# Kernel optimization log

Hardware: AMD Instinct MI355X
Metric: run time of the kernel (lower is better)

The kernel has to match this reference:

```python
import jax, jax.numpy as jnp
import numpy as np

D_MODEL = 1024
N_HEADS = 16
D_K = D_MODEL // N_HEADS
THETA = 10000.0


def _rope(x, token_positions):
    # x: [b, h, s, d_k]; interleaved RoPE (pairs at even/odd positions)
    half = D_K // 2
    inv_freq = 1.0 / (THETA ** (2.0 * jnp.arange(half, dtype=jnp.float32) / D_K))  # [half]
    angles = token_positions.astype(jnp.float32)[:, None] * inv_freq[None, :]      # [s, half]
    sin, cos = jnp.sin(angles), jnp.cos(angles)
    x_even = x[..., 0::2]
    x_odd = x[..., 1::2]
    out_even = cos * x_even - sin * x_odd
    out_odd = sin * x_even + cos * x_odd
    # interleave back: [..., half, 2] -> [..., d_k]
    return jnp.stack((out_even, out_odd), axis=-1).reshape(x.shape)


def setup_inputs() -> dict:
    key = jax.random.key(0)
    kx, kq, kk, kv, ko = jax.random.split(key, 5)
    b, s = 4, 2048
    std = (2.0 / (D_MODEL + D_MODEL)) ** 0.5
    return {
        "x": jax.random.normal(kx, (b, s, D_MODEL), dtype=jnp.float32),
        "Wq": jax.random.normal(kq, (D_MODEL, D_MODEL), dtype=jnp.float32) * std,
        "Wk": jax.random.normal(kk, (D_MODEL, D_MODEL), dtype=jnp.float32) * std,
        "Wv": jax.random.normal(kv, (D_MODEL, D_MODEL), dtype=jnp.float32) * std,
        "Wo": jax.random.normal(ko, (D_MODEL, D_MODEL), dtype=jnp.float32) * std,
        "token_positions": jnp.arange(s, dtype=jnp.int32),
    }


def reference(x, Wq, Wk, Wv, Wo, token_positions):
    b, s, _ = x.shape
    split = lambda t: t.reshape(b, s, N_HEADS, D_K).transpose(0, 2, 1, 3)  # b h s d
    q = split(x @ Wq.T)
    k = split(x @ Wk.T)
    v = split(x @ Wv.T)
    q = _rope(q, token_positions)
    k = _rope(k, token_positions)
    scores = jnp.einsum("bhnd,bhmd->bhnm", q, k) / jnp.sqrt(jnp.float32(D_K))
    causal = jnp.tril(jnp.ones((s, s), dtype=bool))
    scores = jnp.where(causal, scores, -jnp.inf)
    attn = jax.nn.softmax(scores, axis=-1)
    out = jnp.einsum("bhnm,bhmd->bhnd", attn, v)
    out = out.transpose(0, 2, 1, 3).reshape(b, s, D_MODEL)
    return out @ Wo.T
```

## Files before the change

### kernel.cpp

```cpp
#include <hip/hip_runtime.h>
#include <stdint.h>

typedef __attribute__((ext_vector_type(8))) __bf16 bf16x8;
typedef __attribute__((ext_vector_type(4))) float f32x4;
typedef __attribute__((ext_vector_type(16))) float f32x16;
typedef __attribute__((ext_vector_type(8))) unsigned short ushort8;

__device__ __forceinline__ unsigned short f2bf(float f){
  union { float f; unsigned int i; } v; v.f = f;
  unsigned int r = v.i + 0x7fffu + ((v.i >> 16) & 1u);
  return (unsigned short)(r >> 16);
}
__device__ __forceinline__ void gload16(const void* g, void* l){
  __builtin_amdgcn_global_load_lds((__attribute__((address_space(1))) void*)(g),
                                   (__attribute__((address_space(3))) void*)(l),
                                   16, 0, 0);
}
__device__ __forceinline__ unsigned int cvtpk(float lo, float hi){
  unsigned int r;
  asm("v_cvt_pk_bf16_f32 %0, %1, %2" : "=v"(r) : "v"(lo), "v"(hi));
  return r;
}
__device__ __forceinline__ float fexp2(float x){
  float r; asm("v_exp_f32 %0, %1" : "=v"(r) : "v"(x)); return r;
}
__device__ __forceinline__ bf16x8 ldsw(const char* tile, int row, int colb){
  return *(const bf16x8*)(tile + row*128 + (colb ^ ((row & 7) << 4)));
}

#define SEQ   2048
#define DM    1024
#define NH    16
#define DK    64
#define BATCH 4
#define MTOT  (BATCH*SEQ)
#define NX    (MTOT*DM)
#define NW    (DM*DM)

#define QSCALE 0.18033688011112f

__global__ __launch_bounds__(256) void k_tables(const int* __restrict__ pos,
                                                float* __restrict__ tab)
{
  const int idx = blockIdx.x * 256 + threadIdx.x;
  const int s = idx >> 5, i = idx & 31;
  const float inv = __expf(-0.28782313662425575f * (float)i);
  const float a = (float)pos[s] * inv;
  tab[2*idx]   = cosf(a);
  tab[2*idx+1] = sinf(a);
}

__global__ __launch_bounds__(256) void k_convert(
    const float* __restrict__ x,  const float* __restrict__ wq,
    const float* __restrict__ wk, const float* __restrict__ wv,
    const float* __restrict__ wo,
    unsigned short* __restrict__ xb, unsigned short* __restrict__ wb)
{
  const int tid = blockIdx.x * 256 + threadIdx.x;
  const long long e = (long long)tid * 8;
  const float* src; unsigned short* dst;
  if (e < NX) { src = x + e; dst = xb + e; }
  else {
    long long j = e - NX;
    int seg = (int)(j >> 20);
    long long off = j & 1048575;
    src = (seg==0?wq:seg==1?wk:seg==2?wv:wo) + off;
    dst = wb + (size_t)seg*NW + off;
  }
  const float4 a = *(const float4*)src;
  const float4 b = *(const float4*)(src + 4);
  uint4 o;
  o.x = (unsigned int)f2bf(a.x) | ((unsigned int)f2bf(a.y) << 16);
  o.y = (unsigned int)f2bf(a.z) | ((unsigned int)f2bf(a.w) << 16);
  o.z = (unsigned int)f2bf(b.x) | ((unsigned int)f2bf(b.y) << 16);
  o.w = (unsigned int)f2bf(b.z) | ((unsigned int)f2bf(b.w) << 16);
  *(uint4*)dst = o;
}

#define BK64 64
#define NT   (DM/BK64)
#define ABUF 32768
#define BSTRIDE 49152

template<int MODE>
__global__ __launch_bounds__(512, 2) void k_gemm(
    const unsigned short* __restrict__ A,
    const unsigned short* __restrict__ Wb,
    unsigned short* __restrict__ D0,
    unsigned short* __restrict__ D1,
    unsigned short* __restrict__ D2,
    float* __restrict__ Dout,
    const float* __restrict__ tab)
{
  __shared__ __attribute__((aligned(16))) char lds_[3*BSTRIDE];
  const int tid  = threadIdx.x;
  const int lane = tid & 63;
  const int w    = tid >> 6;
  const int wm = w >> 1, wn = w & 1;

  const int bid = blockIdx.x;
  const int tq  = bid >> 3;
  const int m0  = ((bid & 7)*4 + (tq & 3)) * 256;
  const int r   = tq >> 2;
  const int n0  = (MODE == 0 ? (r & 7) : r) * 128;
  const int z   = (MODE == 0) ? (r >> 3) : 0;

  const unsigned short* W = Wb + (size_t)z * NW;
  unsigned short* Dh = (MODE == 0) ? ((z == 0) ? D0 : (z == 1) ? D1 : D2) : nullptr;
  const bool vtr = (MODE == 0) && (z == 2);

  f32x4 acc[4][4];
  #pragma unroll
  for (int i = 0; i < 4; ++i)
    #pragma unroll
    for (int j = 0; j < 4; ++j)
      acc[i][j] = (f32x4)0.0f;

  auto stA = [&](int buf, int t, int l){
    const int k0 = t * BK64;
    const int id = l*512 + tid;
    const int row = id >> 3, c = id & 7;
    gload16(A + (size_t)(m0 + row)*DM + k0 + ((c ^ (row & 7)) << 3),
            lds_ + buf*BSTRIDE + id*16);
  };
  auto stB = [&](int buf, int t, int l){
    const int k0 = t * BK64;
    const int id = l*512 + tid;
    const int row = id >> 3, c = id & 7;
    gload16(W + (size_t)(n0 + row)*DM + k0 + ((c ^ (row & 7)) << 3),
            lds_ + buf*BSTRIDE + ABUF + id*16);
  };
  auto ldA = [&](const char* Ab_, int i, int kk){
    const int row = wm*64 + i*16 + (lane & 15);
    const int c = (kk*4 + (lane >> 4)) ^ (row & 7);
    return *(const bf16x8*)(Ab_ + row*128 + (c << 4));
  };
  auto ldB = [&](const char* Bb_, int j, int kk){
    const int row = wn*64 + j*16 + (lane & 15);
    const int c = (kk*4 + (lane >> 4)) ^ (row & 7);
    return *(const bf16x8*)(Bb_ + row*128 + (c << 4));
  };

  #pragma unroll
  for (int l = 0; l < 4; ++l) stA(0, 0, l);
  stB(0, 0, 0); stB(0, 0, 1);
  #pragma unroll
  for (int l = 0; l < 4; ++l) stA(1, 1, l);
  stB(1, 1, 0); stB(1, 1, 1);
  asm volatile("s_waitcnt vmcnt(6)" ::: "memory");
  __builtin_amdgcn_s_barrier();

  int rb = 0, sb = 2;
  for (int t = 0; t < NT; ++t){
    const char* Ab_ = lds_ + rb*BSTRIDE;
    const char* Bb_ = Ab_ + ABUF;
    const bool st = (t + 2 < NT);
    bf16x8 aF0, aF1, bF[4];

    aF0 = ldA(Ab_, 0, 0); aF1 = ldA(Ab_, 1, 0);
    bF[0] = ldB(Bb_, 0, 0); bF[1] = ldB(Bb_, 1, 0);
    bF[2] = ldB(Bb_, 2, 0); bF[3] = ldB(Bb_, 3, 0);
    if (st){ stA(sb, t+2, 0); stA(sb, t+2, 1); }
    __builtin_amdgcn_s_barrier();
    asm volatile("s_waitcnt lgkmcnt(0)" ::: "memory");
    __builtin_amdgcn_s_setprio(1);
    #pragma unroll
    for (int j = 0; j < 4; ++j){
      acc[0][j] = __builtin_amdgcn_mfma_f32_16x16x32_bf16(aF0, bF[j], acc[0][j], 0, 0, 0);
      acc[1][j] = __builtin_amdgcn_mfma_f32_16x16x32_bf16(aF1, bF[j], acc[1][j], 0, 0, 0);
    }
    __builtin_amdgcn_s_setprio(0);
    __builtin_amdgcn_s_barrier();

    aF0 = ldA(Ab_, 2, 0); aF1 = ldA(Ab_, 3, 0);
    if (st){ stA(sb, t+2, 2); stA(sb, t+2, 3); }
    __builtin_amdgcn_s_barrier();
    asm volatile("s_waitcnt lgkmcnt(0)" ::: "memory");
    __builtin_amdgcn_s_setprio(1);
    #pragma unroll
    for (int j = 0; j < 4; ++j){
      acc[2][j] = __builtin_amdgcn_mfma_f32_16x16x32_bf16(aF0, bF[j], acc[2][j], 0, 0, 0);
      acc[3][j] = __builtin_amdgcn_mfma_f32_16x16x32_bf16(aF1, bF[j], acc[3][j], 0, 0, 0);
    }
    __builtin_amdgcn_s_setprio(0);
    __builtin_amdgcn_s_barrier();

    aF0 = ldA(Ab_, 0, 1); aF1 = ldA(Ab_, 1, 1);
    bF[0] = ldB(Bb_, 0, 1); bF[1] = ldB(Bb_, 1, 1);
    bF[2] = ldB(Bb_, 2, 1); bF[3] = ldB(Bb_, 3, 1);
    if (st){ stB(sb, t+2, 0); stB(sb, t+2, 1); }
    __builtin_amdgcn_s_barrier();
    asm volatile("s_waitcnt lgkmcnt(0)" ::: "memory");
    __builtin_amdgcn_s_setprio(1);
    #pragma unroll
    for (int j = 0; j < 4; ++j){
      acc[0][j] = __builtin_amdgcn_mfma_f32_16x16x32_bf16(aF0, bF[j], acc[0][j], 0, 0, 0);
      acc[1][j] = __builtin_amdgcn_mfma_f32_16x16x32_bf16(aF1, bF[j], acc[1][j], 0, 0, 0);
    }
    __builtin_amdgcn_s_setprio(0);
    __builtin_amdgcn_s_barrier();

    aF0 = ldA(Ab_, 2, 1); aF1 = ldA(Ab_, 3, 1);
    __builtin_amdgcn_s_barrier();
    asm volatile("s_waitcnt lgkmcnt(0)" ::: "memory");
    __builtin_amdgcn_s_setprio(1);
    #pragma unroll
    for (int j = 0; j < 4; ++j){
      acc[2][j] = __builtin_amdgcn_mfma_f32_16x16x32_bf16(aF0, bF[j], acc[2][j], 0, 0, 0);
      acc[3][j] = __builtin_amdgcn_mfma_f32_16x16x32_bf16(aF1, bF[j], acc[3][j], 0, 0, 0);
    }
    __builtin_amdgcn_s_setprio(0);
    if (t < NT-2)       asm volatile("s_waitcnt vmcnt(6)" ::: "memory");
    else if (t == NT-2) asm volatile("s_waitcnt vmcnt(0)" ::: "memory");
    if (t < NT-1) __builtin_amdgcn_s_barrier();

    rb = (rb == 2) ? 0 : rb + 1;
    sb = (sb == 2) ? 0 : sb + 1;
  }

  __syncthreads();

  {
    float* T = (float*)lds_;
    #pragma unroll
    for (int i = 0; i < 4; ++i)
      #pragma unroll
      for (int j = 0; j < 4; ++j){
        const int n = wn*64 + j*16 + (lane & 15);
        #pragma unroll
        for (int rr = 0; rr < 4; ++rr){
          const int m = wm*64 + i*16 + ((lane >> 4) << 2) + rr;
          T[m*128 + (n ^ ((m & 7) << 2))] = acc[i][j][rr];
        }
      }
  }
  __syncthreads();
  const float* T = (const float*)lds_;

  if (MODE == 0 && vtr){
    const int nl = tid >> 2;
    const int sblk = tid & 3;
    const int d = nl & 63, hh = (n0 >> 6) + (nl >> 6);
    const int bidx = m0 >> 11;
    unsigned short* vrow = Dh + (((size_t)(bidx*NH + hh))*DK + d)*SEQ + (m0 & 2047);
    #pragma unroll
    for (int c = 0; c < 8; ++c){
      const int s0 = sblk*8 + c*32;
      float v[8];
      #pragma unroll
      for (int j2 = 0; j2 < 8; ++j2)
        v[j2] = T[(s0 + j2)*128 + (nl ^ (((s0 + j2) & 7) << 2))];
      uint4 ov;
      ov.x = cvtpk(v[0], v[1]); ov.y = cvtpk(v[2], v[3]);
      ov.z = cvtpk(v[4], v[5]); ov.w = cvtpk(v[6], v[7]);
      *(uint4*)(vrow + s0) = ov;
    }
  } else {
    const float scale = (MODE == 0 && z == 0) ? QSCALE : 1.0f;
    #pragma unroll
    for (int k = 0; k < 8; ++k){
      const int cid = k*512 + tid;
      const int d8   = cid & 7;
      const int sp_l = (cid >> 3) & 255;
      const int h    = cid >> 11;
      const int nb   = h*64 + d8*8;
      const int sw   = (sp_l & 7) << 2;
      const f32x4 c0 = *(const f32x4*)&T[sp_l*128 + (nb ^ sw)];
      const f32x4 c1 = *(const f32x4*)&T[sp_l*128 + ((nb + 4) ^ sw)];
      if (MODE == 1){
        float* dst = Dout + (size_t)(m0 + sp_l)*DM + n0 + nb;
        *(f32x4*)dst = c0;
        *(f32x4*)(dst + 4) = c1;
      } else {
        const int mg = m0 + sp_l;
        const int bidx = mg >> 11, sp = mg & 2047;
        const float4 t01 = *(const float4*)&tab[(size_t)sp*64 + d8*8];
        const float4 t23 = *(const float4*)&tab[(size_t)sp*64 + d8*8 + 4];
        const unsigned int u0 = cvtpk((t01.x*c0[0] - t01.y*c0[1])*scale,
                                      (t01.y*c0[0] + t01.x*c0[1])*scale);
        const unsigned int u1 = cvtpk((t01.z*c0[2] - t01.w*c0[3])*scale,
                                      (t01.w*c0[2] + t01.z*c0[3])*scale);
        const unsigned int u2 = cvtpk((t23.x*c1[0] - t23.y*c1[1])*scale,
                                      (t23.y*c1[0] + t23.x*c1[1])*scale);
        const unsigned int u3 = cvtpk((t23.z*c1[2] - t23.w*c1[3])*scale,
                                      (t23.w*c1[2] + t23.z*c1[3])*scale);
        const int hh = (n0 >> 6) + h;
        uint4 ov; ov.x = u0; ov.y = u1; ov.z = u2; ov.w = u3;
        *(uint4*)(Dh + ((size_t)((bidx*NH + hh)*SEQ + sp))*DK + d8*8) = ov;
      }
    }
  }
}

__global__ __launch_bounds__(512, 4) void k_attn(const unsigned short* __restrict__ Qh,
                                                 const unsigned short* __restrict__ Kh,
                                                 const unsigned short* __restrict__ Vt,
                                                 unsigned short* __restrict__ Ab)
{
  __shared__ uint4 ldsu[4096];
  char* base = (char*)ldsu;
  const int tid  = threadIdx.x;
  const int lane = tid & 63;
  const int w    = tid >> 6;
  const int ww   = w & 3;
  const int g    = w >> 2;
  const int tl   = tid & 255;
  const int l31  = lane & 31;
  const int hl   = lane >> 5;
  char* gb = base + g*32768;

  const int jj = blockIdx.x, bh = blockIdx.y;
  const unsigned short* Qb = Qh + (size_t)bh*(SEQ*DK);
  const unsigned short* Kb = Kh + (size_t)bh*(SEQ*DK);
  const unsigned short* Vb = Vt + (size_t)bh*(SEQ*DK);
  const int b = bh >> 4, hd = bh & 15;

  for (int pass = 0; pass < 2; ++pass){
    const int qt = pass ? jj : 15 - jj;
    const int q0 = qt * 128;
    const int qbase = q0 + ww*32;

    bf16x8 qf[4];
    #pragma unroll
    for (int t = 0; t < 4; ++t)
      qf[t] = *(const bf16x8*)(Qb + (size_t)(qbase + l31)*DK + t*16 + hl*8);

    f32x16 acc0 = (f32x16)0.0f, acc1 = (f32x16)0.0f;
    float lsum = 0.0f;

    const int nk = qt + 1;
    const int tbase = g * nk;
    const int wqmax = qbase + 31;

    auto stage = [&](int buf, int ktile){
      const int k0s = ktile * 64;
      char* Kd = gb + buf*16384;
      char* Vd = Kd + 8192;
      #pragma unroll
      for (int cc = 0; cc < 2; ++cc){
        const int f = cc*256 + tl;
        const int r = f >> 3, slot = f & 7;
        const int sw = ((slot ^ (r & 7)) << 3);
        gload16(Kb + (size_t)(k0s + r)*DK + sw, Kd + (cc*256 + ww*64)*16);
        gload16(Vb + (size_t)r*SEQ + k0s + sw, Vd + (cc*256 + ww*64)*16);
      }
    };

    if (pass) __syncthreads();
    stage(0, tbase);
    __syncthreads();
    int cur = 0;

    for (int kt = 0; kt < nk; ++kt){
      const int k0 = (tbase + kt) * 64;
      if (kt + 1 < nk) stage(cur ^ 1, tbase + kt + 1);
      if (k0 <= wqmax){
        const char* Ks = gb + cur*16384;
        const char* Vs = Ks + 8192;

        f32x16 sv0 = (f32x16)0.0f, sv1 = (f32x16)0.0f;
        __builtin_amdgcn_s_setprio(1);
        #pragma unroll
        for (int t = 0; t < 4; ++t){
          const int colb = t*32 + hl*16;
          const bf16x8 a0 = ldsw(Ks, l31, colb);
          const bf16x8 a1 = ldsw(Ks, 32 + l31, colb);
          sv0 = __builtin_amdgcn_mfma_f32_32x32x16_bf16(a0, qf[t], sv0, 0, 0, 0);
          sv1 = __builtin_amdgcn_mfma_f32_32x32x16_bf16(a1, qf[t], sv1, 0, 0, 0);
        }
        __builtin_amdgcn_s_setprio(0);

        if (k0 + 63 > qbase){
          const int q = qbase + l31;
          #pragma unroll
          for (int j = 0; j < 16; ++j){
            const int kv = k0 + (j&3) + 8*(j>>2) + 4*hl;
            if (kv > q)      sv0[j] = -1e30f;
            if (kv + 32 > q) sv1[j] = -1e30f;
          }
        }

        #pragma unroll
        for (int j = 0; j < 16; ++j){
          sv0[j] = fexp2(sv0[j]);
          sv1[j] = fexp2(sv1[j]);
        }
        float ts[8];
        #pragma unroll
        for (int j = 0; j < 8; ++j)
          ts[j] = (sv0[j] + sv0[j+8]) + (sv1[j] + sv1[j+8]);
        #pragma unroll
        for (int off = 4; off; off >>= 1)
          #pragma unroll
          for (int j = 0; j < off; ++j)
            ts[j] += ts[j+off];
        lsum += ts[0] + __shfl_xor(ts[0], 32, 64);

        __builtin_amdgcn_s_setprio(1);
        #pragma unroll
        for (int t = 0; t < 4; ++t){
          f32x16& s = (t < 2) ? sv0 : sv1;
          const int b0v = (t & 1) * 8;
          const unsigned int A0 = cvtpk(s[b0v+0], s[b0v+1]);
          const unsigned int A1 = cvtpk(s[b0v+2], s[b0v+3]);
          const unsigned int B0 = cvtpk(s[b0v+4], s[b0v+5]);
          const unsigned int B1 = cvtpk(s[b0v+6], s[b0v+7]);
          const unsigned int s0 = hl ? A0 : B0;
          const unsigned int s1 = hl ? A1 : B1;
          const unsigned int r0 = (unsigned int)__shfl_xor((int)s0, 32, 64);
          const unsigned int r1 = (unsigned int)__shfl_xor((int)s1, 32, 64);
          union { unsigned int u[4]; bf16x8 v; } f;
          f.u[0] = hl ? r0 : A0; f.u[1] = hl ? r1 : A1;
          f.u[2] = hl ? B0 : r0; f.u[3] = hl ? B1 : r1;
          const int colb = t*32 + hl*16;
          const bf16x8 v0 = ldsw(Vs, l31, colb);
          const bf16x8 v1 = ldsw(Vs, 32 + l31, colb);
          acc0 = __builtin_amdgcn_mfma_f32_32x32x16_bf16(v0, f.v, acc0, 0, 0, 0);
          acc1 = __builtin_amdgcn_mfma_f32_32x32x16_bf16(v1, f.v, acc1, 0, 0, 0);
        }
        __builtin_amdgcn_s_setprio(0);
      }
      __syncthreads();
      cur ^= 1;
    }

    if (g == 1){
      char* cw = base + ww*9216 + lane*144;
      #pragma unroll
      for (int q4 = 0; q4 < 4; ++q4){
        *(f32x4*)(cw + q4*16)      = (f32x4){acc0[4*q4], acc0[4*q4+1], acc0[4*q4+2], acc0[4*q4+3]};
        *(f32x4*)(cw + 64 + q4*16) = (f32x4){acc1[4*q4], acc1[4*q4+1], acc1[4*q4+2], acc1[4*q4+3]};
      }
      *(float*)(cw + 128) = lsum;
    }
    __syncthreads();
    if (g == 0){
      const char* cr = base + ww*9216 + lane*144;
      const float l1 = *(const float*)(cr + 128);
      const float linv = 1.0f / (lsum + l1);
      unsigned short* orow = Ab + ((size_t)(b*SEQ + qbase + l31))*DM + hd*DK;
      #pragma unroll
      for (int mt = 0; mt < 2; ++mt){
        #pragma unroll
        for (int g4 = 0; g4 < 4; ++g4){
          const f32x16& a = mt ? acc1 : acc0;
          const f32x4 o = *(const f32x4*)(cr + mt*64 + g4*16);
          const unsigned int u0 = cvtpk((a[4*g4+0] + o[0])*linv, (a[4*g4+1] + o[1])*linv);
          const unsigned int u1 = cvtpk((a[4*g4+2] + o[2])*linv, (a[4*g4+3] + o[3])*linv);
          *(unsigned long long*)(orow + mt*32 + g4*8 + hl*4) =
              (unsigned long long)u0 | ((unsigned long long)u1 << 32);
        }
      }
    }
  }
}

extern "C" void kernel_launch(void* const* d_in, const int* in_sizes, int n_in,
                              void* d_out, int out_size, void* d_ws, size_t ws_size,
                              hipStream_t stream)
{
  (void)in_sizes; (void)n_in; (void)out_size;
  const float* x  = (const float*)d_in[0];
  const float* wq = (const float*)d_in[1];
  const float* wk = (const float*)d_in[2];
  const float* wv = (const float*)d_in[3];
  const float* wo = (const float*)d_in[4];
  const int* pos  = (const int*)d_in[5];
  float* out = (float*)d_out;

  if (ws_size < 92800000u) return;
  char* ws = (char*)d_ws;
  unsigned short* xb = (unsigned short*)(ws);
  unsigned short* wb = (unsigned short*)(ws + 16777216);
  unsigned short* Qh = (unsigned short*)(ws + 25165824);
  unsigned short* Kh = (unsigned short*)(ws + 41943040);
  unsigned short* Vt = (unsigned short*)(ws + 75497472);
  float* tab         = (float*)(ws + 92274688);

  k_tables  <<<256, 256, 0, stream>>>(pos, tab);
  k_convert <<<6144, 256, 0, stream>>>(x, wq, wk, wv, wo, xb, wb);
  k_gemm<0> <<<768, 512, 0, stream>>>(xb, wb, Qh, Kh, Vt, nullptr, tab);
  k_attn    <<<dim3(8, 64), 512, 0, stream>>>(Qh, Kh, Vt, xb);
  k_gemm<1> <<<256, 512, 0, stream>>>(xb, wb + 3*NW, nullptr, nullptr,
                                      nullptr, out, nullptr);
}
```

Measured before the change: 164.6 us.

## Use larger 256x256 tiles with double buffering for fused QKV projection GEMM

Splits the QKV projection into a dedicated kernel that computes 256x256 output tiles per block with 8 waves in a 2x4 layout. Each wave now holds 8x4 accumulators and the K loop is double-buffered over 128 KB of LDS instead of triple-buffered, which halves the block count to 384 and raises arithmetic intensity per global load. The epilogue is done in two halves to fit the transposed tile in LDS. The costs are one block per CU, higher register pressure and fewer blocks than the 256-CU machine can fill evenly, with a full vmcnt(0) wait each iteration.

```diff
diff --git a/kernel.cpp b/kernel.cpp
--- a/kernel.cpp
+++ b/kernel.cpp
@@ -77,61 +77,55 @@
   *(uint4*)dst = o;
 }
 
-#define BK64 64
-#define NT   (DM/BK64)
-#define ABUF 32768
-#define BSTRIDE 49152
-
-template<int MODE>
-__global__ __launch_bounds__(512, 2) void k_gemm(
+#define G0_NT 16
+#define G0_BSTR 65536
+
+__global__ __launch_bounds__(512) void k_g0(
     const unsigned short* __restrict__ A,
     const unsigned short* __restrict__ Wb,
     unsigned short* __restrict__ D0,
     unsigned short* __restrict__ D1,
     unsigned short* __restrict__ D2,
-    float* __restrict__ Dout,
     const float* __restrict__ tab)
 {
-  __shared__ __attribute__((aligned(16))) char lds_[3*BSTRIDE];
+  __shared__ __attribute__((aligned(16))) char lds_[131072];
   const int tid  = threadIdx.x;
   const int lane = tid & 63;
   const int w    = tid >> 6;
-  const int wm = w >> 1, wn = w & 1;
+  const int wm = w >> 2, wn = w & 3;
 
   const int bid = blockIdx.x;
   const int tq  = bid >> 3;
   const int m0  = ((bid & 7)*4 + (tq & 3)) * 256;
   const int r   = tq >> 2;
-  const int n0  = (MODE == 0 ? (r & 7) : r) * 128;
-  const int z   = (MODE == 0) ? (r >> 3) : 0;
+  const int n0  = (r & 3) * 256;
+  const int z   = r >> 2;
 
   const unsigned short* W = Wb + (size_t)z * NW;
-  unsigned short* Dh = (MODE == 0) ? ((z == 0) ? D0 : (z == 1) ? D1 : D2) : nullptr;
-  const bool vtr = (MODE == 0) && (z == 2);
-
-  f32x4 acc[4][4];
-  #pragma unroll
-  for (int i = 0; i < 4; ++i)
+  unsigned short* Dh = (z == 0) ? D0 : (z == 1) ? D1 : D2;
+  const bool vtr = (z == 2);
+
+  f32x4 acc[8][4];
+  #pragma unroll
+  for (int i = 0; i < 8; ++i)
     #pragma unroll
     for (int j = 0; j < 4; ++j)
       acc[i][j] = (f32x4)0.0f;
 
   auto stA = [&](int buf, int t, int l){
-    const int k0 = t * BK64;
     const int id = l*512 + tid;
     const int row = id >> 3, c = id & 7;
-    gload16(A + (size_t)(m0 + row)*DM + k0 + ((c ^ (row & 7)) << 3),
-            lds_ + buf*BSTRIDE + id*16);
+    gload16(A + (size_t)(m0 + row)*DM + t*64 + ((c ^ (row & 7)) << 3),
+            lds_ + buf*G0_BSTR + id*16);
   };
   auto stB = [&](int buf, int t, int l){
-    const int k0 = t * BK64;
     const int id = l*512 + tid;
     const int row = id >> 3, c = id & 7;
-    gload16(W + (size_t)(n0 + row)*DM + k0 + ((c ^ (row & 7)) << 3),
-            lds_ + buf*BSTRIDE + ABUF + id*16);
+    gload16(W + (size_t)(n0 + row)*DM + t*64 + ((c ^ (row & 7)) << 3),
+            lds_ + buf*G0_BSTR + 32768 + id*16);
   };
   auto ldA = [&](const char* Ab_, int i, int kk){
-    const int row = wm*64 + i*16 + (lane & 15);
+    const int row = wm*128 + i*16 + (lane & 15);
     const int c = (kk*4 + (lane >> 4)) ^ (row & 7);
     return *(const bf16x8*)(Ab_ + row*128 + (c << 4));
   };
@@ -141,141 +135,126 @@
     return *(const bf16x8*)(Bb_ + row*128 + (c << 4));
   };
 
+#define G0_MFMA16(IA, IB)                                                               \
+  _Pragma("unroll")                                                                     \
+  for (int j = 0; j < 4; ++j){                                                          \
+    acc[IA][j] = __builtin_amdgcn_mfma_f32_16x16x32_bf16(aF[0][0], bF[j][0], acc[IA][j], 0, 0, 0); \
+    acc[IA][j] = __builtin_amdgcn_mfma_f32_16x16x32_bf16(aF[0][1], bF[j][1], acc[IA][j], 0, 0, 0); \
+    acc[IB][j] = __builtin_amdgcn_mfma_f32_16x16x32_bf16(aF[1][0], bF[j][0], acc[IB][j], 0, 0, 0); \
+    acc[IB][j] = __builtin_amdgcn_mfma_f32_16x16x32_bf16(aF[1][1], bF[j][1], acc[IB][j], 0, 0, 0); \
+  }
+
   #pragma unroll
   for (int l = 0; l < 4; ++l) stA(0, 0, l);
-  stB(0, 0, 0); stB(0, 0, 1);
-  #pragma unroll
-  for (int l = 0; l < 4; ++l) stA(1, 1, l);
-  stB(1, 1, 0); stB(1, 1, 1);
-  asm volatile("s_waitcnt vmcnt(6)" ::: "memory");
+  #pragma unroll
+  for (int l = 0; l < 4; ++l) stB(0, 0, l);
+  asm volatile("s_waitcnt vmcnt(0)" ::: "memory");
   __builtin_amdgcn_s_barrier();
 
-  int rb = 0, sb = 2;
-  for (int t = 0; t < NT; ++t){
-    const char* Ab_ = lds_ + rb*BSTRIDE;
-    const char* Bb_ = Ab_ + ABUF;
-    const bool st = (t + 2 < NT);
-    bf16x8 aF0, aF1, bF[4];
-
-    aF0 = ldA(Ab_, 0, 0); aF1 = ldA(Ab_, 1, 0);
-    bF[0] = ldB(Bb_, 0, 0); bF[1] = ldB(Bb_, 1, 0);
-    bF[2] = ldB(Bb_, 2, 0); bF[3] = ldB(Bb_, 3, 0);
-    if (st){ stA(sb, t+2, 0); stA(sb, t+2, 1); }
-    __builtin_amdgcn_s_barrier();
-    asm volatile("s_waitcnt lgkmcnt(0)" ::: "memory");
-    __builtin_amdgcn_s_setprio(1);
-    #pragma unroll
-    for (int j = 0; j < 4; ++j){
-      acc[0][j] = __builtin_amdgcn_mfma_f32_16x16x32_bf16(aF0, bF[j], acc[0][j], 0, 0, 0);
-      acc[1][j] = __builtin_amdgcn_mfma_f32_16x16x32_bf16(aF1, bF[j], acc[1][j], 0, 0, 0);
-    }
-    __builtin_amdgcn_s_setprio(0);
-    __builtin_amdgcn_s_barrier();
-
-    aF0 = ldA(Ab_, 2, 0); aF1 = ldA(Ab_, 3, 0);
-    if (st){ stA(sb, t+2, 2); stA(sb, t+2, 3); }
-    __builtin_amdgcn_s_barrier();
-    asm volatile("s_waitcnt lgkmcnt(0)" ::: "memory");
-    __builtin_amdgcn_s_setprio(1);
-    #pragma unroll
-    for (int j = 0; j < 4; ++j){
-      acc[2][j] = __builtin_amdgcn_mfma_f32_16x16x32_bf16(aF0, bF[j], acc[2][j], 0, 0, 0);
-      acc[3][j] = __builtin_amdgcn_mfma_f32_16x16x32_bf16(aF1, bF[j], acc[3][j], 0, 0, 0);
-    }
-    __builtin_amdgcn_s_setprio(0);
-    __builtin_amdgcn_s_barrier();
-
-    aF0 = ldA(Ab_, 0, 1); aF1 = ldA(Ab_, 1, 1);
-    bF[0] = ldB(Bb_, 0, 1); bF[1] = ldB(Bb_, 1, 1);
-    bF[2] = ldB(Bb_, 2, 1); bF[3] = ldB(Bb_, 3, 1);
-    if (st){ stB(sb, t+2, 0); stB(sb, t+2, 1); }
-    __builtin_amdgcn_s_barrier();
-    asm volatile("s_waitcnt lgkmcnt(0)" ::: "memory");
-    __builtin_amdgcn_s_setprio(1);
-    #pragma unroll
-    for (int j = 0; j < 4; ++j){
-      acc[0][j] = __builtin_amdgcn_mfma_f32_16x16x32_bf16(aF0, bF[j], acc[0][j], 0, 0, 0);
-      acc[1][j] = __builtin_amdgcn_mfma_f32_16x16x32_bf16(aF1, bF[j], acc[1][j], 0, 0, 0);
-    }
-    __builtin_amdgcn_s_setprio(0);
-    __builtin_amdgcn_s_barrier();
-
-    aF0 = ldA(Ab_, 2, 1); aF1 = ldA(Ab_, 3, 1);
-    __builtin_amdgcn_s_barrier();
-    asm volatile("s_waitcnt lgkmcnt(0)" ::: "memory");
-    __builtin_amdgcn_s_setprio(1);
-    #pragma unroll
-    for (int j = 0; j < 4; ++j){
-      acc[2][j] = __builtin_amdgcn_mfma_f32_16x16x32_bf16(aF0, bF[j], acc[2][j], 0, 0, 0);
-      acc[3][j] = __builtin_amdgcn_mfma_f32_16x16x32_bf16(aF1, bF[j], acc[3][j], 0, 0, 0);
-    }
-    __builtin_amdgcn_s_setprio(0);
-    if (t < NT-2)       asm volatile("s_waitcnt vmcnt(6)" ::: "memory");
-    else if (t == NT-2) asm volatile("s_waitcnt vmcnt(0)" ::: "memory");
-    if (t < NT-1) __builtin_amdgcn_s_barrier();
-
-    rb = (rb == 2) ? 0 : rb + 1;
-    sb = (sb == 2) ? 0 : sb + 1;
-  }
+  for (int t = 0; t < G0_NT; ++t){
+    const char* Ab_ = lds_ + (t & 1)*G0_BSTR;
+    const char* Bb_ = Ab_ + 32768;
+    const int nb = (t + 1) & 1;
+    const bool st = (t + 1 < G0_NT);
+    bf16x8 aF[2][2], bF[4][2];
+
+    aF[0][0] = ldA(Ab_, 0, 0); aF[0][1] = ldA(Ab_, 0, 1);
+    aF[1][0] = ldA(Ab_, 1, 0); aF[1][1] = ldA(Ab_, 1, 1);
+    #pragma unroll
+    for (int j = 0; j < 4; ++j){ bF[j][0] = ldB(Bb_, j, 0); bF[j][1] = ldB(Bb_, j, 1); }
+    if (st){ stA(nb, t+1, 0); stA(nb, t+1, 1); stA(nb, t+1, 2); stA(nb, t+1, 3); }
+    __builtin_amdgcn_s_barrier();
+    asm volatile("s_waitcnt lgkmcnt(0)" ::: "memory");
+    __builtin_amdgcn_s_setprio(1);
+    G0_MFMA16(0, 1)
+    __builtin_amdgcn_s_setprio(0);
+    __builtin_amdgcn_s_barrier();
+
+    aF[0][0] = ldA(Ab_, 2, 0); aF[0][1] = ldA(Ab_, 2, 1);
+    aF[1][0] = ldA(Ab_, 3, 0); aF[1][1] = ldA(Ab_, 3, 1);
+    if (st){ stB(nb, t+1, 0); stB(nb, t+1, 1); stB(nb, t+1, 2); stB(nb, t+1, 3); }
+    __builtin_amdgcn_s_barrier();
+    asm volatile("s_waitcnt lgkmcnt(0)" ::: "memory");
+    __builtin_amdgcn_s_setprio(1);
+    G0_MFMA16(2, 3)
+    __builtin_amdgcn_s_setprio(0);
+    __builtin_amdgcn_s_barrier();
+
+    aF[0][0] = ldA(Ab_, 4, 0); aF[0][1] = ldA(Ab_, 4, 1);
+    aF[1][0] = ldA(Ab_, 5, 0); aF[1][1] = ldA(Ab_, 5, 1);
+    __builtin_amdgcn_s_barrier();
+    asm volatile("s_waitcnt lgkmcnt(0)" ::: "memory");
+    __builtin_amdgcn_s_setprio(1);
+    G0_MFMA16(4, 5)
+    __builtin_amdgcn_s_setprio(0);
+    __builtin_amdgcn_s_barrier();
+
+    aF[0][0] = ldA(Ab_, 6, 0); aF[0][1] = ldA(Ab_, 6, 1);
+    aF[1][0] = ldA(Ab_, 7, 0); aF[1][1] = ldA(Ab_, 7, 1);
+    __builtin_amdgcn_s_barrier();
+    asm volatile("s_waitcnt lgkmcnt(0)" ::: "memory");
+    __builtin_amdgcn_s_setprio(1);
+    G0_MFMA16(6, 7)
+    __builtin_amdgcn_s_setprio(0);
+    if (st){
+      asm volatile("s_waitcnt vmcnt(0)" ::: "memory");
+      __builtin_amdgcn_s_barrier();
+    }
+  }
+#undef G0_MFMA16
 
   __syncthreads();
-
-  {
-    float* T = (float*)lds_;
-    #pragma unroll
-    for (int i = 0; i < 4; ++i)
+  float* T = (float*)lds_;
+  #pragma unroll
+  for (int h = 0; h < 2; ++h){
+    if (h) __syncthreads();
+    if (wm == h){
       #pragma unroll
-      for (int j = 0; j < 4; ++j){
-        const int n = wn*64 + j*16 + (lane & 15);
-        #pragma unroll
-        for (int rr = 0; rr < 4; ++rr){
-          const int m = wm*64 + i*16 + ((lane >> 4) << 2) + rr;
-          T[m*128 + (n ^ ((m & 7) << 2))] = acc[i][j][rr];
+      for (int i = 0; i < 8; ++i)
+        #pragma unroll
+        for (int j = 0; j < 4; ++j){
+          const int n = wn*64 + j*16 + (lane & 15);
+          #pragma unroll
+          for (int rr = 0; rr < 4; ++rr){
+            const int ml = i*16 + ((lane >> 4) << 2) + rr;
+            T[ml*256 + (n ^ ((ml & 7) << 2))] = acc[i][j][rr];
+          }
         }
+    }
+    __syncthreads();
+    if (vtr){
+      const int nl = tid >> 1, sblk = tid & 1;
+      const int d = nl & 63, hh = (n0 >> 6) + (nl >> 6);
+      const int bidx = m0 >> 11;
+      unsigned short* vrow = Dh + (((size_t)(bidx*NH + hh))*DK + d)*SEQ
+                               + (m0 & 2047) + h*128;
+      #pragma unroll
+      for (int c = 0; c < 8; ++c){
+        const int s0 = sblk*8 + c*16;
+        float v[8];
+        #pragma unroll
+        for (int j2 = 0; j2 < 8; ++j2)
+          v[j2] = T[(s0 + j2)*256 + (nl ^ (((s0 + j2) & 7) << 2))];
+        uint4 ov;
+        ov.x = cvtpk(v[0], v[1]); ov.y = cvtpk(v[2], v[3]);
+        ov.z = cvtpk(v[4], v[5]); ov.w = cvtpk(v[6], v[7]);
+        *(uint4*)(vrow + s0) = ov;
       }
-  }
-  __syncthreads();
-  const float* T = (const float*)lds_;
-
-  if (MODE == 0 && vtr){
-    const int nl = tid >> 2;
-    const int sblk = tid & 3;
-    const int d = nl & 63, hh = (n0 >> 6) + (nl >> 6);
-    const int bidx = m0 >> 11;
-    unsigned short* vrow = Dh + (((size_t)(bidx*NH + hh))*DK + d)*SEQ + (m0 & 2047);
-    #pragma unroll
-    for (int c = 0; c < 8; ++c){
-      const int s0 = sblk*8 + c*32;
-      float v[8];
+    } else {
+      const float scale = (z == 0) ? QSCALE : 1.0f;
       #pragma unroll
-      for (int j2 = 0; j2 < 8; ++j2)
-        v[j2] = T[(s0 + j2)*128 + (nl ^ (((s0 + j2) & 7) << 2))];
-      uint4 ov;
-      ov.x = cvtpk(v[0], v[1]); ov.y = cvtpk(v[2], v[3]);
-      ov.z = cvtpk(v[4], v[5]); ov.w = cvtpk(v[6], v[7]);
-      *(uint4*)(vrow + s0) = ov;
-    }
-  } else {
-    const float scale = (MODE == 0 && z == 0) ? QSCALE : 1.0f;
-    #pragma unroll
-    for (int k = 0; k < 8; ++k){
-      const int cid = k*512 + tid;
-      const int d8   = cid & 7;
-      const int sp_l = (cid >> 3) & 255;
-      const int h    = cid >> 11;
-      const int nb   = h*64 + d8*8;
-      const int sw   = (sp_l & 7) << 2;
-      const f32x4 c0 = *(const f32x4*)&T[sp_l*128 + (nb ^ sw)];
-      const f32x4 c1 = *(const f32x4*)&T[sp_l*128 + ((nb + 4) ^ sw)];
-      if (MODE == 1){
-        float* dst = Dout + (size_t)(m0 + sp_l)*DM + n0 + nb;
-        *(f32x4*)dst = c0;
-        *(f32x4*)(dst + 4) = c1;
-      } else {
-        const int mg = m0 + sp_l;
+      for (int k = 0; k < 8; ++k){
+        const int cid  = k*512 + tid;
+        const int nb2  = (cid & 31) * 8;
+        const int sp_l = cid >> 5;
+        const int sw   = (sp_l & 7) << 2;
+        const f32x4 c0 = *(const f32x4*)&T[sp_l*256 + (nb2 ^ sw)];
+        const f32x4 c1 = *(const f32x4*)&T[sp_l*256 + ((nb2 + 4) ^ sw)];
+        const int mg = m0 + h*128 + sp_l;
         const int bidx = mg >> 11, sp = mg & 2047;
-        const float4 t01 = *(const float4*)&tab[(size_t)sp*64 + d8*8];
-        const float4 t23 = *(const float4*)&tab[(size_t)sp*64 + d8*8 + 4];
+        const int d8 = nb2 & 63;
+        const float4 t01 = *(const float4*)&tab[(size_t)sp*64 + d8];
+        const float4 t23 = *(const float4*)&tab[(size_t)sp*64 + d8 + 4];
         const unsigned int u0 = cvtpk((t01.x*c0[0] - t01.y*c0[1])*scale,
                                       (t01.y*c0[0] + t01.x*c0[1])*scale);
         const unsigned int u1 = cvtpk((t01.z*c0[2] - t01.w*c0[3])*scale,
@@ -284,11 +263,177 @@
                                       (t23.y*c1[0] + t23.x*c1[1])*scale);
         const unsigned int u3 = cvtpk((t23.z*c1[2] - t23.w*c1[3])*scale,
                                       (t23.w*c1[2] + t23.z*c1[3])*scale);
-        const int hh = (n0 >> 6) + h;
+        const int hh = (n0 >> 6) + (nb2 >> 6);
         uint4 ov; ov.x = u0; ov.y = u1; ov.z = u2; ov.w = u3;
-        *(uint4*)(Dh + ((size_t)((bidx*NH + hh)*SEQ + sp))*DK + d8*8) = ov;
+        *(uint4*)(Dh + ((size_t)((bidx*NH + hh)*SEQ + sp))*DK + d8) = ov;
       }
     }
+  }
+}
+
+#define BK64 64
+#define NT   (DM/BK64)
+#define ABUF 32768
+#define BSTRIDE 49152
+
+template<int MODE>
+__global__ __launch_bounds__(512, 2) void k_gemm(
+    const unsigned short* __restrict__ A,
+    const unsigned short* __restrict__ Wb,
+    float* __restrict__ Dout)
+{
+  __shared__ __attribute__((aligned(16))) char lds_[3*BSTRIDE];
+  const int tid  = threadIdx.x;
+  const int lane = tid & 63;
+  const int w    = tid >> 6;
+  const int wm = w >> 1, wn = w & 1;
+
+  const int bid = blockIdx.x;
+  const int tq  = bid >> 3;
+  const int m0  = ((bid & 7)*4 + (tq & 3)) * 256;
+  const int n0  = (tq >> 2) * 128;
+
+  const unsigned short* W = Wb;
+
+  f32x4 acc[4][4];
+  #pragma unroll
+  for (int i = 0; i < 4; ++i)
+    #pragma unroll
+    for (int j = 0; j < 4; ++j)
+      acc[i][j] = (f32x4)0.0f;
+
+  auto stA = [&](int buf, int t, int l){
+    const int k0 = t * BK64;
+    const int id = l*512 + tid;
+    const int row = id >> 3, c = id & 7;
+    gload16(A + (size_t)(m0 + row)*DM + k0 + ((c ^ (row & 7)) << 3),
+            lds_ + buf*BSTRIDE + id*16);
+  };
+  auto stB = [&](int buf, int t, int l){
+    const int k0 = t * BK64;
+    const int id = l*512 + tid;
+    const int row = id >> 3, c = id & 7;
+    gload16(W + (size_t)(n0 + row)*DM + k0 + ((c ^ (row & 7)) << 3),
+            lds_ + buf*BSTRIDE + ABUF + id*16);
+  };
+  auto ldA = [&](const char* Ab_, int i, int kk){
+    const int row = wm*64 + i*16 + (lane & 15);
+    const int c = (kk*4 + (lane >> 4)) ^ (row & 7);
+    return *(const bf16x8*)(Ab_ + row*128 + (c << 4));
+  };
+  auto ldB = [&](const char* Bb_, int j, int kk){
+    const int row = wn*64 + j*16 + (lane & 15);
+    const int c = (kk*4 + (lane >> 4)) ^ (row & 7);
+    return *(const bf16x8*)(Bb_ + row*128 + (c << 4));
+  };
+
+  #pragma unroll
+  for (int l = 0; l < 4; ++l) stA(0, 0, l);
+  stB(0, 0, 0); stB(0, 0, 1);
+  #pragma unroll
+  for (int l = 0; l < 4; ++l) stA(1, 1, l);
+  stB(1, 1, 0); stB(1, 1, 1);
+  asm volatile("s_waitcnt vmcnt(6)" ::: "memory");
+  __builtin_amdgcn_s_barrier();
+
+  int rb = 0, sb = 2;
+  for (int t = 0; t < NT; ++t){
+    const char* Ab_ = lds_ + rb*BSTRIDE;
+    const char* Bb_ = Ab_ + ABUF;
+    const bool st = (t + 2 < NT);
+    bf16x8 aF0, aF1, bF[4];
+
+    aF0 = ldA(Ab_, 0, 0); aF1 = ldA(Ab_, 1, 0);
+    bF[0] = ldB(Bb_, 0, 0); bF[1] = ldB(Bb_, 1, 0);
+    bF[2] = ldB(Bb_, 2, 0); bF[3] = ldB(Bb_, 3, 0);
+    if (st){ stA(sb, t+2, 0); stA(sb, t+2, 1); }
+    __builtin_amdgcn_s_barrier();
+    asm volatile("s_waitcnt lgkmcnt(0)" ::: "memory");
+    __builtin_amdgcn_s_setprio(1);
+    #pragma unroll
+    for (int j = 0; j < 4; ++j){
+      acc[0][j] = __builtin_amdgcn_mfma_f32_16x16x32_bf16(aF0, bF[j], acc[0][j], 0, 0, 0);
+      acc[1][j] = __builtin_amdgcn_mfma_f32_16x16x32_bf16(aF1, bF[j], acc[1][j], 0, 0, 0);
+    }
+    __builtin_amdgcn_s_setprio(0);
+    __builtin_amdgcn_s_barrier();
+
+    aF0 = ldA(Ab_, 2, 0); aF1 = ldA(Ab_, 3, 0);
+    if (st){ stA(sb, t+2, 2); stA(sb, t+2, 3); }
+    __builtin_amdgcn_s_barrier();
+    asm volatile("s_waitcnt lgkmcnt(0)" ::: "memory");
+    __builtin_amdgcn_s_setprio(1);
+    #pragma unroll
+    for (int j = 0; j < 4; ++j){
+      acc[2][j] = __builtin_amdgcn_mfma_f32_16x16x32_bf16(aF0, bF[j], acc[2][j], 0, 0, 0);
+      acc[3][j] = __builtin_amdgcn_mfma_f32_16x16x32_bf16(aF1, bF[j], acc[3][j], 0, 0, 0);
+    }
+    __builtin_amdgcn_s_setprio(0);
+    __builtin_amdgcn_s_barrier();
+
+    aF0 = ldA(Ab_, 0, 1); aF1 = ldA(Ab_, 1, 1);
+    bF[0] = ldB(Bb_, 0, 1); bF[1] = ldB(Bb_, 1, 1);
+    bF[2] = ldB(Bb_, 2, 1); bF[3] = ldB(Bb_, 3, 1);
+    if (st){ stB(sb, t+2, 0); stB(sb, t+2, 1); }
+    __builtin_amdgcn_s_barrier();
+    asm volatile("s_waitcnt lgkmcnt(0)" ::: "memory");
+    __builtin_amdgcn_s_setprio(1);
+    #pragma unroll
+    for (int j = 0; j < 4; ++j){
+      acc[0][j] = __builtin_amdgcn_mfma_f32_16x16x32_bf16(aF0, bF[j], acc[0][j], 0, 0, 0);
+      acc[1][j] = __builtin_amdgcn_mfma_f32_16x16x32_bf16(aF1, bF[j], acc[1][j], 0, 0, 0);
+    }
+    __builtin_amdgcn_s_setprio(0);
+    __builtin_amdgcn_s_barrier();
+
+    aF0 = ldA(Ab_, 2, 1); aF1 = ldA(Ab_, 3, 1);
+    __builtin_amdgcn_s_barrier();
+    asm volatile("s_waitcnt lgkmcnt(0)" ::: "memory");
+    __builtin_amdgcn_s_setprio(1);
+    #pragma unroll
+    for (int j = 0; j < 4; ++j){
+      acc[2][j] = __builtin_amdgcn_mfma_f32_16x16x32_bf16(aF0, bF[j], acc[2][j], 0, 0, 0);
+      acc[3][j] = __builtin_amdgcn_mfma_f32_16x16x32_bf16(aF1, bF[j], acc[3][j], 0, 0, 0);
+    }
+    __builtin_amdgcn_s_setprio(0);
+    if (t < NT-2)       asm volatile("s_waitcnt vmcnt(6)" ::: "memory");
+    else if (t == NT-2) asm volatile("s_waitcnt vmcnt(0)" ::: "memory");
+    if (t < NT-1) __builtin_amdgcn_s_barrier();
+
+    rb = (rb == 2) ? 0 : rb + 1;
+    sb = (sb == 2) ? 0 : sb + 1;
+  }
+
+  __syncthreads();
+  {
+    float* T = (float*)lds_;
+    #pragma unroll
+    for (int i = 0; i < 4; ++i)
+      #pragma unroll
+      for (int j = 0; j < 4; ++j){
+        const int n = wn*64 + j*16 + (lane & 15);
+        #pragma unroll
+        for (int rr = 0; rr < 4; ++rr){
+          const int m = wm*64 + i*16 + ((lane >> 4) << 2) + rr;
+          T[m*128 + (n ^ ((m & 7) << 2))] = acc[i][j][rr];
+        }
+      }
+  }
+  __syncthreads();
+  const float* T = (const float*)lds_;
+  #pragma unroll
+  for (int k = 0; k < 8; ++k){
+    const int cid = k*512 + tid;
+    const int d8   = cid & 7;
+    const int sp_l = (cid >> 3) & 255;
+    const int h    = cid >> 11;
+    const int nb   = h*64 + d8*8;
+    const int sw   = (sp_l & 7) << 2;
+    const f32x4 c0 = *(const f32x4*)&T[sp_l*128 + (nb ^ sw)];
+    const f32x4 c1 = *(const f32x4*)&T[sp_l*128 + ((nb + 4) ^ sw)];
+    float* dst = Dout + (size_t)(m0 + sp_l)*DM + n0 + nb;
+    *(f32x4*)dst = c0;
+    *(f32x4*)(dst + 4) = c1;
   }
 }
 
@@ -479,8 +624,7 @@
 
   k_tables  <<<256, 256, 0, stream>>>(pos, tab);
   k_convert <<<6144, 256, 0, stream>>>(x, wq, wk, wv, wo, xb, wb);
-  k_gemm<0> <<<768, 512, 0, stream>>>(xb, wb, Qh, Kh, Vt, nullptr, tab);
+  k_g0      <<<384, 512, 0, stream>>>(xb, wb, Qh, Kh, Vt, tab);
   k_attn    <<<dim3(8, 64), 512, 0, stream>>>(Qh, Kh, Vt, xb);
-  k_gemm<1> <<<256, 512, 0, stream>>>(xb, wb + 3*NW, nullptr, nullptr,
-                                      nullptr, out, nullptr);
-}
+  k_gemm<1> <<<256, 512, 0, stream>>>(xb, wb + 3*NW, out);
+}
```

New measurement: 168.3 us. +2.3%, slower.
